# Performance work log

Hardware: AMD Instinct MI355X
Metric: run time of the kernel (lower is better)

## Reference

```python
import jax, jax.numpy as jnp
import numpy as np

N_NODES = 100000
N_EDGES = 3200000
D_IN = 256
D_OUT = 256


def setup_inputs() -> dict:
    key = jax.random.key(0)
    k1, k2, k3, k4, k5 = jax.random.split(key, 5)
    x = jax.random.normal(k1, (N_NODES, D_IN), dtype=jnp.float32)
    # xavier-uniform-like init for weight
    limit = float(np.sqrt(6.0 / (D_IN + D_OUT)))
    weight = jax.random.uniform(k2, (D_IN, D_OUT), dtype=jnp.float32, minval=-limit, maxval=limit)
    edge_val = jax.random.uniform(k3, (N_EDGES,), dtype=jnp.float32)
    edge_row = jax.random.randint(k4, (N_EDGES,), 0, N_NODES, dtype=jnp.int32)
    edge_col = jax.random.randint(k5, (N_EDGES,), 0, N_NODES, dtype=jnp.int32)
    return {"x": x, "weight": weight, "edge_val": edge_val,
            "edge_row": edge_row, "edge_col": edge_col}


def reference(x, weight, edge_val, edge_row, edge_col):
    # dropout p=0.0 -> identity
    support = x @ weight                                  # [N, D_OUT]
    # spmm: out[r] += val * support[c] for each edge (r, c, val)
    msgs = support[edge_col] * edge_val[:, None]          # [E, D_OUT]
    out = jax.ops.segment_sum(msgs, edge_row, num_segments=N_NODES)
    return jax.nn.relu(out)
```

## Files before the change

### kernel.cpp

```cpp
#include <hip/hip_runtime.h>

#define N_NODES 100000
#define N_EDGES 3200000
#define D 256
#define CAP 64
#define OVF_MAX 8192

#define BUILD_BLOCKS 3125
#define CAST_BLOCKS 6250
#define GEMM_BLOCKS (N_NODES / 16)

typedef __attribute__((ext_vector_type(8))) short bf16x8;
typedef __attribute__((ext_vector_type(4))) float f32x4;

__device__ unsigned short g_wtp[(size_t)16 * 8 * 64 * 8];
__device__ unsigned short g_xb[(size_t)N_NODES * D];
__device__ unsigned       g_y[(size_t)N_NODES * (D / 2)];
__device__ int   g_cursor[N_NODES];
__device__ int2  g_pad[(size_t)N_NODES * CAP];
__device__ int   g_novf;
__device__ int   g_ovf_row[OVF_MAX];
__device__ int2  g_ovf_edge[OVF_MAX];

__device__ __forceinline__ unsigned short f2bf(float f) {
    unsigned u = __float_as_uint(f);
    unsigned r = u + 0x7fffu + ((u >> 16) & 1u);
    return (unsigned short)(r >> 16);
}

__global__ void setup_kernel(const float* __restrict__ W) {
    const int tid = threadIdx.x;
    if (blockIdx.x < 64) {
        int pb = (blockIdx.x * 256 + tid) * 4;
        #pragma unroll
        for (int j = 0; j < 4; ++j) {
            int p    = pb + j;
            int i8   = p & 7;
            int lane = (p >> 3) & 63;
            int s    = (p >> 9) & 7;
            int nt   = p >> 12;
            int n = nt * 16 + (lane & 15);
            int k = s * 32 + (lane >> 4) * 8 + i8;
            g_wtp[p] = f2bf(W[(size_t)k * D + n]);
        }
    }
    for (int i = blockIdx.x * blockDim.x + tid; i < N_NODES;
         i += gridDim.x * blockDim.x)
        g_cursor[i] = 0;
    if (blockIdx.x == 0 && tid == 0) g_novf = 0;
}

__launch_bounds__(256)
__global__ void build_cast_kernel(const float* __restrict__ x,
                                  const float* __restrict__ edge_val,
                                  const int* __restrict__ edge_row,
                                  const int* __restrict__ edge_col) {
    const int tid = threadIdx.x;
    const int b = blockIdx.x;

    if (b < BUILD_BLOCKS) {
        const int e0 = b * 1024;
        #pragma unroll
        for (int j = 0; j < 4; ++j) {
            int e = e0 + j * 256 + tid;
            int r = edge_row[e];
            int c = edge_col[e];
            float v = edge_val[e];
            int slot = atomicAdd(&g_cursor[r], 1);
            int2 pk; pk.x = c; pk.y = __float_as_int(v);
            if (slot < CAP) {
                g_pad[(size_t)r * CAP + slot] = pk;
            } else {
                int o = atomicAdd(&g_novf, 1);
                if (o < OVF_MAX) { g_ovf_row[o] = r; g_ovf_edge[o] = pk; }
            }
        }
    } else {
        const size_t base = (size_t)(b - BUILD_BLOCKS) * 4096 + (size_t)tid * 16;
        const float4* xp = (const float4*)&x[base];
        float4 f0 = xp[0], f1 = xp[1], f2 = xp[2], f3 = xp[3];
        unsigned short o[16];
        o[ 0]=f2bf(f0.x); o[ 1]=f2bf(f0.y); o[ 2]=f2bf(f0.z); o[ 3]=f2bf(f0.w);
        o[ 4]=f2bf(f1.x); o[ 5]=f2bf(f1.y); o[ 6]=f2bf(f1.z); o[ 7]=f2bf(f1.w);
        o[ 8]=f2bf(f2.x); o[ 9]=f2bf(f2.y); o[10]=f2bf(f2.z); o[11]=f2bf(f2.w);
        o[12]=f2bf(f3.x); o[13]=f2bf(f3.y); o[14]=f2bf(f3.z); o[15]=f2bf(f3.w);
        uint4* dst = (uint4*)&g_xb[base];
        dst[0] = *(const uint4*)&o[0];
        dst[1] = *(const uint4*)&o[8];
    }
}

__launch_bounds__(128)
__global__ void spmm_kernel() {
    const int r = blockIdx.x;
    const int t = threadIdx.x;
    const int deg = g_cursor[r];
    const int dpad = min(deg, CAP);
    const long long* rowp = (const long long*)&g_pad[(size_t)r * CAP];
    const unsigned* xb = (const unsigned*)g_xb;

    float a0 = 0.f, a1 = 0.f;
    int i = 0;
    for (; i + 3 < dpad; i += 4) {
        long long q0 = __builtin_nontemporal_load(&rowp[i]);
        long long q1 = __builtin_nontemporal_load(&rowp[i + 1]);
        long long q2 = __builtin_nontemporal_load(&rowp[i + 2]);
        long long q3 = __builtin_nontemporal_load(&rowp[i + 3]);
        unsigned p0 = xb[(size_t)(int)q0 * (D / 2) + t];
        unsigned p1 = xb[(size_t)(int)q1 * (D / 2) + t];
        unsigned p2 = xb[(size_t)(int)q2 * (D / 2) + t];
        unsigned p3 = xb[(size_t)(int)q3 * (D / 2) + t];
        float v0 = __int_as_float((int)(q0 >> 32));
        float v1 = __int_as_float((int)(q1 >> 32));
        float v2 = __int_as_float((int)(q2 >> 32));
        float v3 = __int_as_float((int)(q3 >> 32));
        a0 += v0 * __uint_as_float(p0 << 16);
        a1 += v0 * __uint_as_float(p0 & 0xffff0000u);
        a0 += v1 * __uint_as_float(p1 << 16);
        a1 += v1 * __uint_as_float(p1 & 0xffff0000u);
        a0 += v2 * __uint_as_float(p2 << 16);
        a1 += v2 * __uint_as_float(p2 & 0xffff0000u);
        a0 += v3 * __uint_as_float(p3 << 16);
        a1 += v3 * __uint_as_float(p3 & 0xffff0000u);
    }
    for (; i < dpad; ++i) {
        long long q0 = __builtin_nontemporal_load(&rowp[i]);
        float v0 = __int_as_float((int)(q0 >> 32));
        unsigned p0 = xb[(size_t)(int)q0 * (D / 2) + t];
        a0 += v0 * __uint_as_float(p0 << 16);
        a1 += v0 * __uint_as_float(p0 & 0xffff0000u);
    }
    const int novf = min(g_novf, OVF_MAX);
    if (novf > 0) {
        for (int j = 0; j < novf; ++j) {
            if (g_ovf_row[j] == r) {
                int2 e0 = g_ovf_edge[j];
                float v0 = __int_as_float(e0.y);
                unsigned p0 = xb[(size_t)e0.x * (D / 2) + t];
                a0 += v0 * __uint_as_float(p0 << 16);
                a1 += v0 * __uint_as_float(p0 & 0xffff0000u);
            }
        }
    }
    g_y[(size_t)r * (D / 2) + t] =
        (unsigned)f2bf(a0) | ((unsigned)f2bf(a1) << 16);
}

__launch_bounds__(256)
__global__ void gemm_kernel(float* __restrict__ out) {
    __shared__ float tile[4][16][68];
    const int g    = blockIdx.x;
    const int wave = threadIdx.x >> 6;
    const int lane = threadIdx.x & 63;
    const int m0   = g * 16;
    const int n0   = wave * 64;
    const int lm   = lane & 15;
    const int q    = lane >> 4;

    const unsigned short* Yb = (const unsigned short*)g_y;
    f32x4 acc0 = {}, acc1 = {}, acc2 = {}, acc3 = {};

    #pragma unroll
    for (int s = 0; s < 8; ++s) {
        bf16x8 av = *(const bf16x8*)&Yb[(size_t)(m0 + lm) * D + s * 32 + q * 8];
        const unsigned short* bp =
            &g_wtp[((size_t)(wave * 4) * 8 + s) * 512 + lane * 8];
        bf16x8 b0 = *(const bf16x8*)&bp[0 * 4096];
        bf16x8 b1 = *(const bf16x8*)&bp[1 * 4096];
        bf16x8 b2 = *(const bf16x8*)&bp[2 * 4096];
        bf16x8 b3 = *(const bf16x8*)&bp[3 * 4096];
        acc0 = __builtin_amdgcn_mfma_f32_16x16x32_bf16(av, b0, acc0, 0, 0, 0);
        acc1 = __builtin_amdgcn_mfma_f32_16x16x32_bf16(av, b1, acc1, 0, 0, 0);
        acc2 = __builtin_amdgcn_mfma_f32_16x16x32_bf16(av, b2, acc2, 0, 0, 0);
        acc3 = __builtin_amdgcn_mfma_f32_16x16x32_bf16(av, b3, acc3, 0, 0, 0);
    }

    #pragma unroll
    for (int r = 0; r < 4; ++r) {
        tile[wave][q * 4 + r][ 0 + lm] = acc0[r];
        tile[wave][q * 4 + r][16 + lm] = acc1[r];
        tile[wave][q * 4 + r][32 + lm] = acc2[r];
        tile[wave][q * 4 + r][48 + lm] = acc3[r];
    }
    const int row  = lane >> 2;
    const int cseg = (lane & 3) * 16;
    float ov[16];
    #pragma unroll
    for (int j = 0; j < 16; ++j)
        ov[j] = fmaxf(tile[wave][row][cseg + j], 0.f);
    float* dst = &out[(size_t)(m0 + row) * D + n0 + cseg];
    #pragma unroll
    for (int j = 0; j < 4; ++j)
        __builtin_nontemporal_store(*(const f32x4*)&ov[j * 4], (f32x4*)&dst[j * 4]);
}

extern "C" void kernel_launch(void* const* d_in, const int* in_sizes, int n_in,
                              void* d_out, int out_size, void* d_ws, size_t ws_size,
                              hipStream_t stream) {
    const float* x        = (const float*)d_in[0];
    const float* weight   = (const float*)d_in[1];
    const float* edge_val = (const float*)d_in[2];
    const int*   edge_row = (const int*)d_in[3];
    const int*   edge_col = (const int*)d_in[4];
    float* out = (float*)d_out;

    setup_kernel<<<64, 256, 0, stream>>>(weight);
    build_cast_kernel<<<BUILD_BLOCKS + CAST_BLOCKS, 256, 0, stream>>>(
        x, edge_val, edge_row, edge_col);
    spmm_kernel<<<N_NODES, 128, 0, stream>>>();
    gemm_kernel<<<GEMM_BLOCKS, 256, 0, stream>>>(out);
}
```

Measured before the change: 667.9 us.

## Replace global-atomic edge scatter with two-pass shared-memory bucket binning

Builds the padded per-row edge lists in two passes. First, edges are counting-sorted into 98 buckets of 1024 rows using shared-memory histograms and block-level reservations. Then one block per bucket scatters its edges into row slots with shared-memory atomics and writes row degrees. This replaces per-edge global atomics and random scatter writes with more local traffic, at the cost of an extra pass over the edges and a low-parallelism second stage of 98 blocks. Scratch buffers now come from the workspace when it is large enough.

```diff
diff --git a/kernel.cpp b/kernel.cpp
--- a/kernel.cpp
+++ b/kernel.cpp
@@ -6,7 +6,12 @@
 #define CAP 64
 #define OVF_MAX 8192
 
-#define BUILD_BLOCKS 3125
+#define NB1 98
+#define RPB1 1024
+#define CAPB1 34816
+#define CHUNK 6144
+#define NBLK_A ((N_EDGES + CHUNK - 1) / CHUNK)
+
 #define CAST_BLOCKS 6250
 #define GEMM_BLOCKS (N_NODES / 16)
 
@@ -14,13 +19,16 @@
 typedef __attribute__((ext_vector_type(4))) float f32x4;
 
 __device__ unsigned short g_wtp[(size_t)16 * 8 * 64 * 8];
-__device__ unsigned short g_xb[(size_t)N_NODES * D];
-__device__ unsigned       g_y[(size_t)N_NODES * (D / 2)];
 __device__ int   g_cursor[N_NODES];
-__device__ int2  g_pad[(size_t)N_NODES * CAP];
+__device__ int   g_b1cur[NB1];
 __device__ int   g_novf;
 __device__ int   g_ovf_row[OVF_MAX];
 __device__ int2  g_ovf_edge[OVF_MAX];
+
+__device__ unsigned short g_xb_fb[(size_t)N_NODES * D];
+__device__ unsigned       g_y_fb[(size_t)N_NODES * (D / 2)];
+__device__ int2           g_pad_fb[(size_t)N_NODES * CAP];
+__device__ int2           g_binned_fb[(size_t)NB1 * CAPB1];
 
 __device__ __forceinline__ unsigned short f2bf(float f) {
     unsigned u = __float_as_uint(f);
@@ -44,60 +52,135 @@
             g_wtp[p] = f2bf(W[(size_t)k * D + n]);
         }
     }
-    for (int i = blockIdx.x * blockDim.x + tid; i < N_NODES;
-         i += gridDim.x * blockDim.x)
-        g_cursor[i] = 0;
-    if (blockIdx.x == 0 && tid == 0) g_novf = 0;
+    if (blockIdx.x == 0) {
+        if (tid < NB1) g_b1cur[tid] = 0;
+        if (tid == 0) g_novf = 0;
+    }
 }
 
 __launch_bounds__(256)
-__global__ void build_cast_kernel(const float* __restrict__ x,
-                                  const float* __restrict__ edge_val,
-                                  const int* __restrict__ edge_row,
-                                  const int* __restrict__ edge_col) {
+__global__ void binA_kernel(const float* __restrict__ edge_val,
+                            const int* __restrict__ edge_row,
+                            const int* __restrict__ edge_col,
+                            int2* __restrict__ binned) {
+    __shared__ int2 rec[CHUNK];
+    __shared__ unsigned char bid[CHUNK];
+    __shared__ int cnt[NB1];
+    __shared__ int pre[NB1 + 1];
+    __shared__ int bas[NB1];
+    const int tid = threadIdx.x;
+    const int e0 = blockIdx.x * CHUNK;
+
+    for (int k = tid; k < NB1; k += 256) cnt[k] = 0;
+    __syncthreads();
+    #pragma unroll
+    for (int j = 0; j < CHUNK / 256; ++j) {
+        int e = e0 + tid + j * 256;
+        if (e < N_EDGES) atomicAdd(&cnt[edge_row[e] >> 10], 1);
+    }
+    __syncthreads();
+    if (tid == 0) {
+        int run = 0;
+        for (int k = 0; k < NB1; ++k) { pre[k] = run; run += cnt[k]; }
+        pre[NB1] = run;
+    }
+    __syncthreads();
+    for (int k = tid; k < NB1; k += 256)
+        bas[k] = cnt[k] ? atomicAdd(&g_b1cur[k], cnt[k]) : 0;
+    __syncthreads();
+    for (int k = tid; k < NB1; k += 256) cnt[k] = 0;
+    __syncthreads();
+    #pragma unroll
+    for (int j = 0; j < CHUNK / 256; ++j) {
+        int e = e0 + tid + j * 256;
+        if (e < N_EDGES) {
+            int r = edge_row[e];
+            int k = r >> 10;
+            int o = atomicAdd(&cnt[k], 1);
+            int pos = pre[k] + o;
+            int2 pk;
+            pk.x = edge_col[e] | ((r & 1023) << 17);
+            pk.y = __float_as_int(edge_val[e]);
+            rec[pos] = pk;
+            bid[pos] = (unsigned char)k;
+        }
+    }
+    __syncthreads();
+    const int total = pre[NB1];
+    for (int i = tid; i < total; i += 256) {
+        int k = bid[i];
+        int dest = bas[k] + (i - pre[k]);
+        int2 pk = rec[i];
+        if (dest < CAPB1) {
+            binned[(size_t)k * CAPB1 + dest] = pk;
+        } else {
+            int o = atomicAdd(&g_novf, 1);
+            if (o < OVF_MAX) {
+                g_ovf_row[o] = (k << 10) | (pk.x >> 17);
+                int2 ov; ov.x = pk.x & 0x1FFFF; ov.y = pk.y;
+                g_ovf_edge[o] = ov;
+            }
+        }
+    }
+}
+
+__launch_bounds__(256)
+__global__ void binB_cast_kernel(const float* __restrict__ x,
+                                 const int2* __restrict__ binned,
+                                 int2* __restrict__ pad,
+                                 unsigned short* __restrict__ xb) {
+    __shared__ int cur[RPB1];
     const int tid = threadIdx.x;
     const int b = blockIdx.x;
 
-    if (b < BUILD_BLOCKS) {
-        const int e0 = b * 1024;
+    if (b < NB1) {
+        for (int i = tid; i < RPB1; i += 256) cur[i] = 0;
+        __syncthreads();
+        const int n = min(g_b1cur[b], CAPB1);
+        const int2* src = &binned[(size_t)b * CAPB1];
+        for (int i = tid; i < n; i += 256) {
+            int2 pk = src[i];
+            int rl  = pk.x >> 17;
+            int col = pk.x & 0x1FFFF;
+            int slot = atomicAdd(&cur[rl], 1);
+            int row = (b << 10) + rl;
+            int2 o2; o2.x = col; o2.y = pk.y;
+            if (slot < CAP) {
+                pad[(size_t)row * CAP + slot] = o2;
+            } else {
+                int o = atomicAdd(&g_novf, 1);
+                if (o < OVF_MAX) { g_ovf_row[o] = row; g_ovf_edge[o] = o2; }
+            }
+        }
+        __syncthreads();
+        for (int i = tid; i < RPB1; i += 256) {
+            int row = (b << 10) + i;
+            if (row < N_NODES) g_cursor[row] = cur[i];
+        }
+    } else {
+        const size_t blockBase = (size_t)(b - NB1) * 4096;
         #pragma unroll
         for (int j = 0; j < 4; ++j) {
-            int e = e0 + j * 256 + tid;
-            int r = edge_row[e];
-            int c = edge_col[e];
-            float v = edge_val[e];
-            int slot = atomicAdd(&g_cursor[r], 1);
-            int2 pk; pk.x = c; pk.y = __float_as_int(v);
-            if (slot < CAP) {
-                g_pad[(size_t)r * CAP + slot] = pk;
-            } else {
-                int o = atomicAdd(&g_novf, 1);
-                if (o < OVF_MAX) { g_ovf_row[o] = r; g_ovf_edge[o] = pk; }
-            }
-        }
-    } else {
-        const size_t base = (size_t)(b - BUILD_BLOCKS) * 4096 + (size_t)tid * 16;
-        const float4* xp = (const float4*)&x[base];
-        float4 f0 = xp[0], f1 = xp[1], f2 = xp[2], f3 = xp[3];
-        unsigned short o[16];
-        o[ 0]=f2bf(f0.x); o[ 1]=f2bf(f0.y); o[ 2]=f2bf(f0.z); o[ 3]=f2bf(f0.w);
-        o[ 4]=f2bf(f1.x); o[ 5]=f2bf(f1.y); o[ 6]=f2bf(f1.z); o[ 7]=f2bf(f1.w);
-        o[ 8]=f2bf(f2.x); o[ 9]=f2bf(f2.y); o[10]=f2bf(f2.z); o[11]=f2bf(f2.w);
-        o[12]=f2bf(f3.x); o[13]=f2bf(f3.y); o[14]=f2bf(f3.z); o[15]=f2bf(f3.w);
-        uint4* dst = (uint4*)&g_xb[base];
-        dst[0] = *(const uint4*)&o[0];
-        dst[1] = *(const uint4*)&o[8];
+            size_t idx = blockBase + (size_t)(j * 256 + tid) * 4;
+            float4 f = *(const float4*)&x[idx];
+            unsigned short o[4];
+            o[0] = f2bf(f.x); o[1] = f2bf(f.y);
+            o[2] = f2bf(f.z); o[3] = f2bf(f.w);
+            *(uint2*)&xb[idx] = *(const uint2*)o;
+        }
     }
 }
 
 __launch_bounds__(128)
-__global__ void spmm_kernel() {
+__global__ void spmm_kernel(const int2* __restrict__ pad,
+                            const unsigned short* __restrict__ xbp,
+                            unsigned* __restrict__ y) {
     const int r = blockIdx.x;
     const int t = threadIdx.x;
     const int deg = g_cursor[r];
     const int dpad = min(deg, CAP);
-    const long long* rowp = (const long long*)&g_pad[(size_t)r * CAP];
-    const unsigned* xb = (const unsigned*)g_xb;
+    const long long* rowp = (const long long*)&pad[(size_t)r * CAP];
+    const unsigned* xb = (const unsigned*)xbp;
 
     float a0 = 0.f, a1 = 0.f;
     int i = 0;
@@ -142,12 +225,13 @@
             }
         }
     }
-    g_y[(size_t)r * (D / 2) + t] =
+    y[(size_t)r * (D / 2) + t] =
         (unsigned)f2bf(a0) | ((unsigned)f2bf(a1) << 16);
 }
 
 __launch_bounds__(256)
-__global__ void gemm_kernel(float* __restrict__ out) {
+__global__ void gemm_kernel(const unsigned short* __restrict__ Yb,
+                            float* __restrict__ out) {
     __shared__ float tile[4][16][68];
     const int g    = blockIdx.x;
     const int wave = threadIdx.x >> 6;
@@ -157,7 +241,6 @@
     const int lm   = lane & 15;
     const int q    = lane >> 4;
 
-    const unsigned short* Yb = (const unsigned short*)g_y;
     f32x4 acc0 = {}, acc1 = {}, acc2 = {}, acc3 = {};
 
     #pragma unroll
@@ -194,6 +277,12 @@
         __builtin_nontemporal_store(*(const f32x4*)&ov[j * 4], (f32x4*)&dst[j * 4]);
 }
 
+#define XB_BYTES   ((size_t)N_NODES * D * 2)
+#define Y_BYTES    ((size_t)N_NODES * D * 2)
+#define PAD_BYTES  ((size_t)N_NODES * CAP * 8)
+#define BIN_BYTES  ((size_t)NB1 * CAPB1 * 8)
+#define ALIGNUP(v) (((v) + 255) & ~(size_t)255)
+
 extern "C" void kernel_launch(void* const* d_in, const int* in_sizes, int n_in,
                               void* d_out, int out_size, void* d_ws, size_t ws_size,
                               hipStream_t stream) {
@@ -204,9 +293,33 @@
     const int*   edge_col = (const int*)d_in[4];
     float* out = (float*)d_out;
 
+    static void* s_xb = nullptr; static void* s_y = nullptr;
+    static void* s_pad = nullptr; static void* s_bin = nullptr;
+    if (!s_xb) {
+        hipGetSymbolAddress(&s_xb,  HIP_SYMBOL(g_xb_fb));
+        hipGetSymbolAddress(&s_y,   HIP_SYMBOL(g_y_fb));
+        hipGetSymbolAddress(&s_pad, HIP_SYMBOL(g_pad_fb));
+        hipGetSymbolAddress(&s_bin, HIP_SYMBOL(g_binned_fb));
+    }
+    unsigned short* xb;  unsigned* y;  int2* pad;  int2* binned;
+    const size_t need = ALIGNUP(XB_BYTES) + ALIGNUP(Y_BYTES) +
+                        ALIGNUP(PAD_BYTES) + ALIGNUP(BIN_BYTES);
+    if (d_ws && ws_size >= need) {
+        char* p = (char*)d_ws;
+        xb     = (unsigned short*)p; p += ALIGNUP(XB_BYTES);
+        y      = (unsigned*)p;       p += ALIGNUP(Y_BYTES);
+        pad    = (int2*)p;           p += ALIGNUP(PAD_BYTES);
+        binned = (int2*)p;
+    } else {
+        xb     = (unsigned short*)s_xb;
+        y      = (unsigned*)s_y;
+        pad    = (int2*)s_pad;
+        binned = (int2*)s_bin;
+    }
+
     setup_kernel<<<64, 256, 0, stream>>>(weight);
-    build_cast_kernel<<<BUILD_BLOCKS + CAST_BLOCKS, 256, 0, stream>>>(
-        x, edge_val, edge_row, edge_col);
-    spmm_kernel<<<N_NODES, 128, 0, stream>>>();
-    gemm_kernel<<<GEMM_BLOCKS, 256, 0, stream>>>(out);
-}
+    binA_kernel<<<NBLK_A, 256, 0, stream>>>(edge_val, edge_row, edge_col, binned);
+    binB_cast_kernel<<<NB1 + CAST_BLOCKS, 256, 0, stream>>>(x, binned, pad, xb);
+    spmm_kernel<<<N_NODES, 128, 0, stream>>>(pad, xb, y);
+    gemm_kernel<<<GEMM_BLOCKS, 256, 0, stream>>>((const unsigned short*)y, out);
+}
```

New measurement: 623.6 us. -6.6%, faster.
